# Kernel tuning notes

Measured on AMD Instinct MI355X. Metric: run time of the kernel, lower is better.

## Reference

```python
import jax, jax.numpy as jnp
import numpy as np

BETA = 1e10  # hard softmax temperature from the original module


def setup_inputs() -> dict:
    key = jax.random.key(0)
    ks = jax.random.split(key, 7)
    bs, nc, units, feat = 128, 1024, 512, 512
    return {
        "x": jax.random.normal(ks[0], (bs, feat), jnp.float32),
        "class_logits": jax.random.normal(ks[1], (bs, nc), jnp.float32),
        "h_states": jax.random.normal(ks[2], (nc, units), jnp.float32) * 0.1,
        "c_states": jax.random.normal(ks[3], (nc, units), jnp.float32) * 0.1,
        "kernel": jax.random.normal(ks[4], (feat, 4 * units), jnp.float32) * 0.05,
        "rec_kernel": jax.random.normal(ks[5], (units, 4 * units), jnp.float32) * 0.05,
        "bias": jnp.zeros((4 * units,), jnp.float32),
    }


def _diff_scatter(A, B, w):
    # A: (nc, u) old class states, B: (bs, u) new states, w: (bs, nc) hard softmax.
    # Faithful to tf version: broadcast to (nc, bs, u), blend, then reduce_max over bs.
    m = w.T[:, :, None]                       # (nc, bs, 1)
    blended = A[:, None, :] * (1.0 - m) + B[None, :, :] * m  # (nc, bs, u)
    return jnp.max(blended, axis=1)           # (nc, u)


def reference(x, class_logits, h_states, c_states, kernel, rec_kernel, bias):
    # diff_gather: softmax-weighted sum over classes == weights @ params
    w = jax.nn.softmax(class_logits * BETA, axis=-1)  # (bs, nc), ~one-hot
    h0 = w @ h_states                                  # (bs, u)
    c0 = w @ c_states                                  # (bs, u)

    # single-step Keras LSTM (seq_len == 1): gate order i, f, c, o
    z = x @ kernel + h0 @ rec_kernel + bias            # (bs, 4u)
    i, f, g, o = jnp.split(z, 4, axis=-1)
    i = jax.nn.sigmoid(i)
    f = jax.nn.sigmoid(f)
    g = jnp.tanh(g)
    o = jax.nn.sigmoid(o)
    c = f * c0 + i * g
    h = o * jnp.tanh(c)                                # LSTM output == h

    new_h = _diff_scatter(h_states, h, w)
    new_c = _diff_scatter(c_states, c, w)
    return h, new_h, new_c
```

## Files before the change

### kernel.cpp

```cpp
#include <hip/hip_runtime.h>
#include <hip/hip_bf16.h>
#include <math.h>

#define BS    128
#define NC    1024
#define UNITS 512
#define FEAT  512
#define FOURU 2048
#define KG    4
#define NT    16

typedef short bf16x8 __attribute__((ext_vector_type(8)));
typedef float f32x4  __attribute__((ext_vector_type(4)));

__device__ __forceinline__ unsigned short bf_rhu(float f) {
    union { float f; unsigned u; } v; v.f = f;
    return (unsigned short)((v.u + 0x8000u) >> 16);
}
__device__ __forceinline__ unsigned pack2(float a, float b) {
    return (unsigned)bf_rhu(a) | ((unsigned)bf_rhu(b) << 16);
}

__global__ __launch_bounds__(256) void argmax_prep_kernel(
    const float* __restrict__ logits, const float* __restrict__ x,
    const float* __restrict__ h_states,
    int* __restrict__ sidx, unsigned* __restrict__ Abf )
{
    int b = blockIdx.x;
    int t = threadIdx.x;
    float best = -INFINITY; int bi = 0;
    for (int i = t; i < NC; i += 256) {
        float v = logits[b * NC + i];
        if (v > best) { best = v; bi = i; }
    }
    for (int off = 32; off > 0; off >>= 1) {
        float ov = __shfl_down(best, off);
        int   oi = __shfl_down(bi, off);
        if (ov > best || (ov == best && oi < bi)) { best = ov; bi = oi; }
    }
    __shared__ float sv[4]; __shared__ int si[4]; __shared__ int sbi;
    int wid = t >> 6;
    if ((t & 63) == 0) { sv[wid] = best; si[wid] = bi; }
    __syncthreads();
    if (t == 0) {
        for (int w = 1; w < 4; ++w)
            if (sv[w] > best || (sv[w] == best && si[w] < bi)) { best = sv[w]; bi = si[w]; }
        sidx[b] = bi;
        sbi = bi;
    }
    __syncthreads();
    int st = t & 127;
    const float* srcrow = (t < 128) ? (x + (long)b * FEAT)
                                    : (h_states + (long)sbi * UNITS);
    float4 v = *(const float4*)(srcrow + st * 4);
    unsigned lo = pack2(v.x, v.y), hi = pack2(v.z, v.w);
    unsigned du = (unsigned)b * 512u + (t < 128 ? 0u : 256u) + (unsigned)st * 2u;
    *(uint2*)(Abf + du) = make_uint2(lo, hi);
}

__global__ __launch_bounds__(256) void gemm_kernel(
    const unsigned short* __restrict__ Abf,
    const float* __restrict__ kern, const float* __restrict__ reck,
    float* __restrict__ z_part)
{
    const int t = threadIdx.x;
    const int wid = t >> 6, lane = t & 63, l15 = lane & 15, quad = lane >> 4;
    const int nt = blockIdx.x, kg = blockIdx.y;
    const int n  = nt * NT + l15;
    const int k0base = kg * 256;
    const float* W  = (kg < 2) ? kern : reck;
    const int wkbase = (kg & 1) * 256;

    f32x4 zero = {0.f, 0.f, 0.f, 0.f};
    f32x4 acc[2] = {zero, zero};

    #pragma unroll
    for (int kstep = 0; kstep < 8; ++kstep) {
        int k0  = k0base + kstep * 32 + quad * 8;
        int wk0 = wkbase + kstep * 32 + quad * 8;

        bf16x8 af[2], wf;
        #pragma unroll
        for (int ms = 0; ms < 2; ++ms) {
            int m = wid * 32 + ms * 16 + l15;
            af[ms] = *(const bf16x8*)(Abf + (long)m * 1024 + k0);
        }
        const float* Wp = W + (long)wk0 * FOURU + n;
        #pragma unroll
        for (int j = 0; j < 8; ++j)
            wf[j] = (short)bf_rhu(Wp[(long)j * FOURU]);

        #pragma unroll
        for (int ms = 0; ms < 2; ++ms)
            acc[ms] = __builtin_amdgcn_mfma_f32_16x16x32_bf16(af[ms], wf, acc[ms], 0, 0, 0);
    }

    float* zp = z_part + (long)kg * BS * FOURU;
    #pragma unroll
    for (int ms = 0; ms < 2; ++ms)
        #pragma unroll
        for (int r = 0; r < 4; ++r) {
            int m = wid * 32 + ms * 16 + quad * 4 + r;
            zp[(long)m * FOURU + n] = acc[ms][r];
        }
}

__global__ __launch_bounds__(256) void scatter_lstm_kernel(
    const float* __restrict__ z_part, const float* __restrict__ bias,
    const float* __restrict__ h_states, const float* __restrict__ c_states,
    const int* __restrict__ sidx,
    float* __restrict__ h_out, float* __restrict__ out_h, float* __restrict__ out_c)
{
    __shared__ int s[BS];
    int t = threadIdx.x;
    if (t < BS) s[t] = sidx[t];
    __syncthreads();
    int j = blockIdx.x >> 1;
    int u = (blockIdx.x & 1) * 256 + t;

    float ah = h_states[(long)j * UNITS + u];
    float ac = c_states[(long)j * UNITS + u];

    float mh = -INFINITY, mc = -INFINITY;
    int count = 0;
    float bi_ = bias[u], bf_ = bias[512 + u], bg_ = bias[1024 + u], bo_ = bias[1536 + u];

    for (int b = 0; b < BS; ++b) {
        if (s[b] == j) {
            ++count;
            float zi = bi_, zf = bf_, zg = bg_, zo = bo_;
            #pragma unroll
            for (int kg = 0; kg < KG; ++kg) {
                const float* zp = z_part + (long)kg * BS * FOURU + (long)b * FOURU;
                zi += zp[u];
                zf += zp[512 + u];
                zg += zp[1024 + u];
                zo += zp[1536 + u];
            }
            float ig = 1.f / (1.f + expf(-zi));
            float fg = 1.f / (1.f + expf(-zf));
            float gg = tanhf(zg);
            float og = 1.f / (1.f + expf(-zo));
            float c  = fg * ac + ig * gg;
            float h  = og * tanhf(c);
            h_out[(long)b * UNITS + u] = h;
            mh = fmaxf(mh, h);
            mc = fmaxf(mc, c);
        }
    }
    out_h[(long)j * UNITS + u] = (count == BS) ? mh : fmaxf(ah, mh);
    out_c[(long)j * UNITS + u] = (count == BS) ? mc : fmaxf(ac, mc);
}

extern "C" void kernel_launch(void* const* d_in, const int* in_sizes, int n_in,
                              void* d_out, int out_size, void* d_ws, size_t ws_size,
                              hipStream_t stream)
{
    (void)in_sizes; (void)n_in; (void)out_size; (void)ws_size;
    const float* x      = (const float*)d_in[0];
    const float* logits = (const float*)d_in[1];
    const float* h_st   = (const float*)d_in[2];
    const float* c_st   = (const float*)d_in[3];
    const float* kern   = (const float*)d_in[4];
    const float* reck   = (const float*)d_in[5];
    const float* bias   = (const float*)d_in[6];

    float* out        = (float*)d_out;
    float* out_h_step = out;
    float* out_newh   = out + BS * UNITS;
    float* out_newc   = out + BS * UNITS + NC * UNITS;

    char*           ws     = (char*)d_ws;
    int*            sidx   = (int*)ws;
    unsigned*       Abf    = (unsigned*)(ws + 4096);
    float*          z_part = (float*)(ws + (1u << 20));

    argmax_prep_kernel<<<BS, 256, 0, stream>>>(logits, x, h_st, sidx, Abf);
    gemm_kernel<<<dim3(128, KG), 256, 0, stream>>>(
        (const unsigned short*)Abf, kern, reck, z_part);
    scatter_lstm_kernel<<<NC * UNITS / 256, 256, 0, stream>>>(
        z_part, bias, h_st, c_st, sidx, out_h_step, out_newh, out_newc);
}
```

Before: 102.2 us.

## Fuse argmax and bf16 conversion into GEMM, halve K split partials

Removes the separate argmax/prep kernel. The GEMM blocks now convert x and the gathered h_states rows to bf16 on the fly, and the recurrent-half blocks compute the per-row argmax redundantly before their MFMA loop. The K split drops from four partials to two (input vs recurrent), so each block runs 16 k-steps over 64 rows, and the scatter kernel sums two partials with 512-thread blocks, one per class. This saves a launch and a workspace round trip at the cost of redundant logits reads (each recurrent block rescans 64 rows) and less GEMM parallelism per block.

```diff
diff --git a/kernel.cpp b/kernel.cpp
--- a/kernel.cpp
+++ b/kernel.cpp
@@ -1,5 +1,4 @@
 #include <hip/hip_runtime.h>
-#include <hip/hip_bf16.h>
 #include <math.h>
 
 #define BS    128
@@ -7,8 +6,6 @@
 #define UNITS 512
 #define FEAT  512
 #define FOURU 2048
-#define KG    4
-#define NT    16
 
 typedef short bf16x8 __attribute__((ext_vector_type(8)));
 typedef float f32x4  __attribute__((ext_vector_type(4)));
@@ -17,96 +14,94 @@
     union { float f; unsigned u; } v; v.f = f;
     return (unsigned short)((v.u + 0x8000u) >> 16);
 }
-__device__ __forceinline__ unsigned pack2(float a, float b) {
-    return (unsigned)bf_rhu(a) | ((unsigned)bf_rhu(b) << 16);
-}
 
-__global__ __launch_bounds__(256) void argmax_prep_kernel(
-    const float* __restrict__ logits, const float* __restrict__ x,
+__global__ __launch_bounds__(256) void gemm_fused_kernel(
+    const float* __restrict__ logits,
+    const float* __restrict__ x,
     const float* __restrict__ h_states,
-    int* __restrict__ sidx, unsigned* __restrict__ Abf )
+    const float* __restrict__ kern,
+    const float* __restrict__ reck,
+    int*   __restrict__ sidx,
+    float* __restrict__ z)
 {
-    int b = blockIdx.x;
-    int t = threadIdx.x;
-    float best = -INFINITY; int bi = 0;
-    for (int i = t; i < NC; i += 256) {
-        float v = logits[b * NC + i];
-        if (v > best) { best = v; bi = i; }
+    const int t    = threadIdx.x;
+    const int wid  = t >> 6, lane = t & 63, l15 = lane & 15, quad = lane >> 4;
+    const int bid  = blockIdx.x;
+    const bool isrec = bid >= 256;
+    const int lb   = isrec ? bid - 256 : bid;
+    const int nt   = lb >> 1, mh = lb & 1;
+    const int n    = nt * 16 + l15;
+    const int mbase = mh * 64;
+
+    __shared__ int smax[64];
+
+    if (isrec) {
+        int r = mbase + (t >> 2);
+        int q = t & 3;
+        const float* lp = logits + (long)r * NC + q * 256;
+        float best = -INFINITY; int bi = 0;
+        #pragma unroll 4
+        for (int i = 0; i < 256; i += 4) {
+            float4 v = *(const float4*)(lp + i);
+            int base = q * 256 + i;
+            if (v.x > best) { best = v.x; bi = base; }
+            if (v.y > best) { best = v.y; bi = base + 1; }
+            if (v.z > best) { best = v.z; bi = base + 2; }
+            if (v.w > best) { best = v.w; bi = base + 3; }
+        }
+        #pragma unroll
+        for (int m = 1; m <= 2; m <<= 1) {
+            float ov = __shfl_xor(best, m);
+            int   oi = __shfl_xor(bi, m);
+            if (ov > best || (ov == best && oi < bi)) { best = ov; bi = oi; }
+        }
+        if (q == 0) smax[t >> 2] = bi;
+        __syncthreads();
+        if (nt == 0 && t < 64) sidx[mbase + t] = smax[t];
     }
-    for (int off = 32; off > 0; off >>= 1) {
-        float ov = __shfl_down(best, off);
-        int   oi = __shfl_down(bi, off);
-        if (ov > best || (ov == best && oi < bi)) { best = ov; bi = oi; }
+
+    const float* W = isrec ? reck : kern;
+    const float* A;
+    long abase;
+    if (isrec) {
+        A = h_states;
+        abase = (long)smax[wid * 16 + l15] * UNITS;
+    } else {
+        A = x;
+        abase = (long)(mbase + wid * 16 + l15) * FEAT;
     }
-    __shared__ float sv[4]; __shared__ int si[4]; __shared__ int sbi;
-    int wid = t >> 6;
-    if ((t & 63) == 0) { sv[wid] = best; si[wid] = bi; }
-    __syncthreads();
-    if (t == 0) {
-        for (int w = 1; w < 4; ++w)
-            if (sv[w] > best || (sv[w] == best && si[w] < bi)) { best = sv[w]; bi = si[w]; }
-        sidx[b] = bi;
-        sbi = bi;
-    }
-    __syncthreads();
-    int st = t & 127;
-    const float* srcrow = (t < 128) ? (x + (long)b * FEAT)
-                                    : (h_states + (long)sbi * UNITS);
-    float4 v = *(const float4*)(srcrow + st * 4);
-    unsigned lo = pack2(v.x, v.y), hi = pack2(v.z, v.w);
-    unsigned du = (unsigned)b * 512u + (t < 128 ? 0u : 256u) + (unsigned)st * 2u;
-    *(uint2*)(Abf + du) = make_uint2(lo, hi);
-}
 
-__global__ __launch_bounds__(256) void gemm_kernel(
-    const unsigned short* __restrict__ Abf,
-    const float* __restrict__ kern, const float* __restrict__ reck,
-    float* __restrict__ z_part)
-{
-    const int t = threadIdx.x;
-    const int wid = t >> 6, lane = t & 63, l15 = lane & 15, quad = lane >> 4;
-    const int nt = blockIdx.x, kg = blockIdx.y;
-    const int n  = nt * NT + l15;
-    const int k0base = kg * 256;
-    const float* W  = (kg < 2) ? kern : reck;
-    const int wkbase = (kg & 1) * 256;
+    f32x4 acc = {0.f, 0.f, 0.f, 0.f};
+    #pragma unroll
+    for (int kstep = 0; kstep < 16; ++kstep) {
+        int k0 = kstep * 32 + quad * 8;
+        float4 a0 = *(const float4*)(A + abase + k0);
+        float4 a1 = *(const float4*)(A + abase + k0 + 4);
+        bf16x8 af;
+        af[0] = (short)bf_rhu(a0.x); af[1] = (short)bf_rhu(a0.y);
+        af[2] = (short)bf_rhu(a0.z); af[3] = (short)bf_rhu(a0.w);
+        af[4] = (short)bf_rhu(a1.x); af[5] = (short)bf_rhu(a1.y);
+        af[6] = (short)bf_rhu(a1.z); af[7] = (short)bf_rhu(a1.w);
 
-    f32x4 zero = {0.f, 0.f, 0.f, 0.f};
-    f32x4 acc[2] = {zero, zero};
-
-    #pragma unroll
-    for (int kstep = 0; kstep < 8; ++kstep) {
-        int k0  = k0base + kstep * 32 + quad * 8;
-        int wk0 = wkbase + kstep * 32 + quad * 8;
-
-        bf16x8 af[2], wf;
-        #pragma unroll
-        for (int ms = 0; ms < 2; ++ms) {
-            int m = wid * 32 + ms * 16 + l15;
-            af[ms] = *(const bf16x8*)(Abf + (long)m * 1024 + k0);
-        }
-        const float* Wp = W + (long)wk0 * FOURU + n;
+        const float* Wp = W + (long)k0 * FOURU + n;
+        bf16x8 wf;
         #pragma unroll
         for (int j = 0; j < 8; ++j)
             wf[j] = (short)bf_rhu(Wp[(long)j * FOURU]);
 
-        #pragma unroll
-        for (int ms = 0; ms < 2; ++ms)
-            acc[ms] = __builtin_amdgcn_mfma_f32_16x16x32_bf16(af[ms], wf, acc[ms], 0, 0, 0);
+        acc = __builtin_amdgcn_mfma_f32_16x16x32_bf16(af, wf, acc, 0, 0, 0);
     }
 
-    float* zp = z_part + (long)kg * BS * FOURU;
+    float* zp = z + (isrec ? (long)BS * FOURU : 0);
     #pragma unroll
-    for (int ms = 0; ms < 2; ++ms)
-        #pragma unroll
-        for (int r = 0; r < 4; ++r) {
-            int m = wid * 32 + ms * 16 + quad * 4 + r;
-            zp[(long)m * FOURU + n] = acc[ms][r];
-        }
+    for (int r2 = 0; r2 < 4; ++r2) {
+        int m = mbase + wid * 16 + quad * 4 + r2;
+        zp[(long)m * FOURU + n] = acc[r2];
+    }
 }
 
-__global__ __launch_bounds__(256) void scatter_lstm_kernel(
-    const float* __restrict__ z_part, const float* __restrict__ bias,
+__global__ __launch_bounds__(512) void scatter_lstm_kernel(
+    const float* __restrict__ z, const float* __restrict__ bias,
     const float* __restrict__ h_states, const float* __restrict__ c_states,
     const int* __restrict__ sidx,
     float* __restrict__ h_out, float* __restrict__ out_h, float* __restrict__ out_c)
@@ -115,8 +110,8 @@
     int t = threadIdx.x;
     if (t < BS) s[t] = sidx[t];
     __syncthreads();
-    int j = blockIdx.x >> 1;
-    int u = (blockIdx.x & 1) * 256 + t;
+    int j = blockIdx.x;
+    int u = t;
 
     float ah = h_states[(long)j * UNITS + u];
     float ac = c_states[(long)j * UNITS + u];
@@ -128,15 +123,12 @@
     for (int b = 0; b < BS; ++b) {
         if (s[b] == j) {
             ++count;
-            float zi = bi_, zf = bf_, zg = bg_, zo = bo_;
-            #pragma unroll
-            for (int kg = 0; kg < KG; ++kg) {
-                const float* zp = z_part + (long)kg * BS * FOURU + (long)b * FOURU;
-                zi += zp[u];
-                zf += zp[512 + u];
-                zg += zp[1024 + u];
-                zo += zp[1536 + u];
-            }
+            const float* z0 = z + (long)b * FOURU;
+            const float* z1 = z + (long)BS * FOURU + (long)b * FOURU;
+            float zi = bi_ + z0[u]        + z1[u];
+            float zf = bf_ + z0[512 + u]  + z1[512 + u];
+            float zg = bg_ + z0[1024 + u] + z1[1024 + u];
+            float zo = bo_ + z0[1536 + u] + z1[1536 + u];
             float ig = 1.f / (1.f + expf(-zi));
             float fg = 1.f / (1.f + expf(-zf));
             float gg = tanhf(zg);
@@ -170,14 +162,11 @@
     float* out_newh   = out + BS * UNITS;
     float* out_newc   = out + BS * UNITS + NC * UNITS;
 
-    char*           ws     = (char*)d_ws;
-    int*            sidx   = (int*)ws;
-    unsigned*       Abf    = (unsigned*)(ws + 4096);
-    float*          z_part = (float*)(ws + (1u << 20));
+    char* ws   = (char*)d_ws;
+    int*  sidx = (int*)ws;
+    float* z   = (float*)(ws + 4096);
 
-    argmax_prep_kernel<<<BS, 256, 0, stream>>>(logits, x, h_st, sidx, Abf);
-    gemm_kernel<<<dim3(128, KG), 256, 0, stream>>>(
-        (const unsigned short*)Abf, kern, reck, z_part);
-    scatter_lstm_kernel<<<NC * UNITS / 256, 256, 0, stream>>>(
-        z_part, bias, h_st, c_st, sidx, out_h_step, out_newh, out_newc);
+    gemm_fused_kernel<<<512, 256, 0, stream>>>(logits, x, h_st, kern, reck, sidx, z);
+    scatter_lstm_kernel<<<NC, 512, 0, stream>>>(
+        z, bias, h_st, c_st, sidx, out_h_step, out_newh, out_newc);
 }
```

Result: slower. 112.9 us (+10.6%).
